# Kernel tuning notes

Hardware: AMD Instinct MI355X
Metric: run time of the kernel (lower is better)

Reference implementation:

```python
import jax, jax.numpy as jnp
import numpy as np

N = 100000
E = 1600000


def setup_inputs() -> dict:
    key = jax.random.key(0)
    ks = jax.random.split(key, 8)
    x = jax.random.normal(ks[0], (N, 4), dtype=jnp.float32)
    edge_index = jax.random.randint(ks[1], (2, E), 0, N)
    # Glorot-ish scaled weights
    W1 = jax.random.normal(ks[2], (4, 64), dtype=jnp.float32) / np.sqrt(4.0)
    b1 = jnp.zeros((64,), dtype=jnp.float32)
    W2 = jax.random.normal(ks[3], (64, 32), dtype=jnp.float32) / np.sqrt(64.0)
    b2 = jnp.zeros((32,), dtype=jnp.float32)
    Wf = jax.random.normal(ks[4], (32, 32), dtype=jnp.float32) / np.sqrt(32.0)
    bf = jnp.zeros((32,), dtype=jnp.float32)
    return {"x": x, "edge_index": edge_index, "W1": W1, "b1": b1,
            "W2": W2, "b2": b2, "Wf": Wf, "bf": bf}


def _gcn_conv(x, W, b, src, dst, n):
    """PyG GCNConv: out = D^{-1/2}(A+I)D^{-1/2} (x @ W) + b, sum-aggregated at dst."""
    h = x @ W  # [n, out] -- linear before propagate, like PyG
    # degree over dst (self-loops already appended in src/dst)
    deg = jax.ops.segment_sum(jnp.ones_like(dst, dtype=h.dtype), dst, num_segments=n)
    dinv = jnp.where(deg > 0, jax.lax.rsqrt(jnp.maximum(deg, 1.0)), 0.0)
    norm = dinv[src] * dinv[dst]  # [E+n]
    msg = h[src] * norm[:, None]  # gather + scale
    out = jax.ops.segment_sum(msg, dst, num_segments=n)  # scatter-add
    return out + b


def reference(x, edge_index, W1, b1, W2, b2, Wf, bf):
    n = x.shape[0]
    loops = jnp.arange(n, dtype=edge_index.dtype)
    src = jnp.concatenate([edge_index[0], loops])
    dst = jnp.concatenate([edge_index[1], loops])
    h = jax.nn.relu(_gcn_conv(x, W1, b1, src, dst, n))
    h = jax.nn.relu(_gcn_conv(h, W2, b2, src, dst, n))
    return jax.nn.relu(h @ Wf + bf)
```

## Files before the change

kernel.cpp:

```cpp
#include <hip/hip_runtime.h>
#include <hip/hip_fp16.h>


#define STRIDE 64
#define BSHIFT 7
#define CH 4096
#define PBS 1024
#define PT (CH / PBS)

__global__ __launch_bounds__(PBS) void k_place(const int* __restrict__ src,
                                               const int* __restrict__ dst,
                                               int* __restrict__ gcur,
                                               int* __restrict__ ebuf,
                                               int NB, int CAP, int E) {
    __shared__ int stage[CH];
    __shared__ unsigned short stageb[CH];
    __shared__ int histA[1024];
    __shared__ int gbaseL[1024];
    __shared__ int wtot[16];
    const int tid = threadIdx.x;
    const int base = blockIdx.x * CH;
    const int blkcnt = min(CH, E - base);

    histA[tid] = 0;
    __syncthreads();

    int posr[PT];
    unsigned short bkr[PT];
    unsigned char lnr[PT];
#pragma unroll
    for (int k = 0; k < PT; ++k) {
        int e = base + tid + k * PBS;
        if (e < E) {
            int d = dst[e];
            int b = d >> BSHIFT;
            bkr[k] = (unsigned short)b;
            lnr[k] = (unsigned char)(d & 127);
            posr[k] = atomicAdd(&histA[b], 1);
        }
    }
    __syncthreads();

    {
        int lane = tid & 63, wid = tid >> 6;
        int v = histA[tid];
#pragma unroll
        for (int o = 1; o < 64; o <<= 1) {
            int t2 = __shfl_up(v, o, 64);
            if (lane >= o) v += t2;
        }
        if (lane == 63) wtot[wid] = v;
        __syncthreads();
        int wpre = 0;
        for (int ww = 0; ww < wid; ++ww) wpre += wtot[ww];
        histA[tid] = v + wpre;
    }
    __syncthreads();

    int* A = histA;

    if (tid < NB) {
        int st = tid ? A[tid - 1] : 0;
        int cnt = A[tid] - st;
        gbaseL[tid] = cnt ? atomicAdd(&gcur[tid], cnt) : 0;
    }
    __syncthreads();

#pragma unroll
    for (int k = 0; k < PT; ++k) {
        int e = base + tid + k * PBS;
        if (e < E) {
            int b = bkr[k];
            int st = b ? A[b - 1] : 0;
            int idx = st + posr[k];
            stage[idx] = src[e] | ((int)lnr[k] << 17);
            stageb[idx] = (unsigned short)b;
        }
    }
    __syncthreads();

    for (int j = tid; j < blkcnt; j += PBS) {
        int b = stageb[j];
        int st = b ? A[b - 1] : 0;
        int o = gbaseL[b] + (j - st);
        if (o < CAP) ebuf[(size_t)b * CAP + o] = stage[j];
    }
}

__global__ __launch_bounds__(512) void k_fillsorted2(const int* __restrict__ ebuf,
                                                     const int* __restrict__ gcur,
                                                     int* __restrict__ adjF,
                                                     int* __restrict__ deg,
                                                     float* __restrict__ dinv,
                                                     const float4* __restrict__ x,
                                                     float4* __restrict__ xd,
                                                     int CAP, int N) {
    __shared__ int adjL[128 * STRIDE];
    __shared__ int cnt[128];
    const int b = blockIdx.x, tid = threadIdx.x;
    if (tid < 128) cnt[tid] = 0;
    __syncthreads();

    int count = min(gcur[b], CAP);
    const int* eb = ebuf + (size_t)b * CAP;
    for (int j = tid; j < count; j += 512) {
        int v = eb[j];
        int ln = (v >> 17) & 127;
        int s = v & 0x1FFFF;
        int slot = atomicAdd(&cnt[ln], 1);
        if (slot < STRIDE) adjL[(ln << 6) | slot] = s;
    }
    __syncthreads();

    const size_t gbase = (size_t)b << 13;
    for (int j = tid; j < 128 * STRIDE; j += 512) adjF[gbase + j] = adjL[j];

    if (tid < 128) {
        int node = (b << BSHIFT) + tid;
        if (node < N) {
            int k = cnt[tid];
            deg[node] = k;
            float di = rsqrtf((float)(k + 1));
            dinv[node] = di;
            float4 xv = x[node];
            xv.x *= di; xv.y *= di; xv.z *= di; xv.w *= di;
            xd[node] = xv;
        }
    }
}

__global__ void k_agg(const int* __restrict__ deg, const int* __restrict__ adjF,
                      const float4* __restrict__ xd, float4* __restrict__ aggx, int n) {
    int hw = blockIdx.x * (blockDim.x >> 5) + (threadIdx.x >> 5);
    int lane = threadIdx.x & 31;
    int sub = lane >> 3;
    int sl  = lane & 7;
    int node = hw * 4 + sub;
    bool valid = node < n;
    int nd = valid ? node : 0;
    int c = valid ? min(deg[nd], STRIDE) : 0;
    const int* row = adjF + ((size_t)nd << 6);

    float ax = 0.f, ay = 0.f, az = 0.f, aw = 0.f;
    int kk = sl;
    for (; kk + 8 < c; kk += 16) {
        int s0 = row[kk], s1 = row[kk + 8];
        float4 v0 = xd[s0];
        float4 v1 = xd[s1];
        ax += v0.x + v1.x; ay += v0.y + v1.y;
        az += v0.z + v1.z; aw += v0.w + v1.w;
    }
    if (kk < c) {
        float4 v = xd[row[kk]];
        ax += v.x; ay += v.y; az += v.z; aw += v.w;
    }
#pragma unroll
    for (int m = 4; m >= 1; m >>= 1) {
        ax += __shfl_xor(ax, m, 8);
        ay += __shfl_xor(ay, m, 8);
        az += __shfl_xor(az, m, 8);
        aw += __shfl_xor(aw, m, 8);
    }
    if (valid && sl == 0) aggx[nd] = make_float4(ax, ay, az, aw);
}

__global__ void k_mlp(const float4* __restrict__ aggx, const float4* __restrict__ xd,
                      const float* __restrict__ dinv,
                      const float* __restrict__ W1, const float* __restrict__ b1,
                      const float* __restrict__ W2, signed char* __restrict__ Qq,
                      float* __restrict__ Qs, int n) {
    int i = blockIdx.x * blockDim.x + threadIdx.x;
    if (i >= n) return;
    float4 s = aggx[i];
    float4 self = xd[i];
    float di = dinv[i];
    float ax = (s.x + self.x) * di, ay = (s.y + self.y) * di;
    float az = (s.z + self.z) * di, aw = (s.w + self.w) * di;

    float r[32];
#pragma unroll
    for (int c = 0; c < 32; ++c) r[c] = 0.0f;

#pragma unroll 8
    for (int j = 0; j < 64; ++j) {
        float h = fmaf(ax, W1[j], fmaf(ay, W1[64 + j],
                  fmaf(az, W1[128 + j], fmaf(aw, W1[192 + j], b1[j]))));
        h = fmaxf(h, 0.0f);
#pragma unroll
        for (int c = 0; c < 32; ++c) r[c] = fmaf(h, W2[j * 32 + c], r[c]);
    }

    float rm = 1e-12f;
#pragma unroll
    for (int c = 0; c < 32; ++c) {
        r[c] *= di;
        rm = fmaxf(rm, fabsf(r[c]));
    }
    float inv = 127.0f / rm;
    unsigned pk[8];
#pragma unroll
    for (int g = 0; g < 8; ++g) {
        unsigned q0 = (unsigned)(__float2int_rn(r[4 * g + 0] * inv)) & 0xFFu;
        unsigned q1 = (unsigned)(__float2int_rn(r[4 * g + 1] * inv)) & 0xFFu;
        unsigned q2 = (unsigned)(__float2int_rn(r[4 * g + 2] * inv)) & 0xFFu;
        unsigned q3 = (unsigned)(__float2int_rn(r[4 * g + 3] * inv)) & 0xFFu;
        pk[g] = q0 | (q1 << 8) | (q2 << 16) | (q3 << 24);
    }
    uint4* qq = (uint4*)(Qq + ((size_t)i << 5));
    qq[0] = make_uint4(pk[0], pk[1], pk[2], pk[3]);
    qq[1] = make_uint4(pk[4], pk[5], pk[6], pk[7]);
    Qs[i] = rm * (1.0f / 127.0f);
}

__global__ void k_final(const int* __restrict__ deg, const int* __restrict__ adjF,
                        const float* __restrict__ dinv,
                        const signed char* __restrict__ Qq,
                        const float* __restrict__ Qs, const float* __restrict__ b2,
                        const float* __restrict__ Wf, const float* __restrict__ bf,
                        float* __restrict__ out, int n) {
    int node = blockIdx.x * (blockDim.x >> 5) + (threadIdx.x >> 5);
    int lane = threadIdx.x & 31;
    bool valid = node < n;
    int nd = valid ? node : 0;
    int c = valid ? min(deg[nd], STRIDE) : 0;
    const int* row = adjF + ((size_t)nd << 6);
    const int nb = lane >> 3;
    const int cw = lane & 7;

    float a0 = 0.f, a1 = 0.f, a2 = 0.f, a3 = 0.f;
    for (int k = 0; k < c; k += 8) {
        int i0 = k + nb, i1 = k + 4 + nb;
        int s0 = row[min(i0, c - 1)];
        int s1 = row[min(i1, c - 1)];
        int w0 = ((const int*)(Qq + ((size_t)s0 << 5)))[cw];
        int w1 = ((const int*)(Qq + ((size_t)s1 << 5)))[cw];
        float sc0 = Qs[s0];
        float sc1 = Qs[s1];
        sc0 = (i0 < c) ? sc0 : 0.0f;
        sc1 = (i1 < c) ? sc1 : 0.0f;
        a0 = fmaf(sc0, (float)((signed char)(w0)), a0);
        a1 = fmaf(sc0, (float)((signed char)(w0 >> 8)), a1);
        a2 = fmaf(sc0, (float)((signed char)(w0 >> 16)), a2);
        a3 = fmaf(sc0, (float)(w0 >> 24), a3);
        a0 = fmaf(sc1, (float)((signed char)(w1)), a0);
        a1 = fmaf(sc1, (float)((signed char)(w1 >> 8)), a1);
        a2 = fmaf(sc1, (float)((signed char)(w1 >> 16)), a2);
        a3 = fmaf(sc1, (float)(w1 >> 24), a3);
    }

    a0 += __shfl_xor(a0, 8, 32);  a0 += __shfl_xor(a0, 16, 32);
    a1 += __shfl_xor(a1, 8, 32);  a1 += __shfl_xor(a1, 16, 32);
    a2 += __shfl_xor(a2, 8, 32);  a2 += __shfl_xor(a2, 16, 32);
    a3 += __shfl_xor(a3, 8, 32);  a3 += __shfl_xor(a3, 16, 32);

    int srcl = lane >> 2;
    float t0 = __shfl(a0, srcl, 32);
    float t1 = __shfl(a1, srcl, 32);
    float t2 = __shfl(a2, srcl, 32);
    float t3 = __shfl(a3, srcl, 32);
    int r2 = lane & 3;
    float accv = (r2 & 1) ? t1 : t0;
    float hi   = (r2 & 1) ? t3 : t2;
    accv = (r2 & 2) ? hi : accv;

    accv += Qs[nd] * (float)Qq[((size_t)nd << 5) | lane];

    float h = fmaxf(fmaf(accv, dinv[nd], b2[lane]), 0.0f);
    float o = bf[lane];
#pragma unroll
    for (int cc = 0; cc < 32; ++cc) {
        o = fmaf(__shfl(h, cc, 32), Wf[cc * 32 + lane], o);
    }
    if (valid) out[((size_t)node << 5) | lane] = fmaxf(o, 0.0f);
}

static inline size_t align_up(size_t x, size_t a) { return (x + a - 1) & ~(a - 1); }

extern "C" void kernel_launch(void* const* d_in, const int* in_sizes, int n_in,
                              void* d_out, int out_size, void* d_ws, size_t ws_size,
                              hipStream_t stream) {
    const int N = in_sizes[0] / 4;
    const int E = in_sizes[1] / 2;

    const float* x  = (const float*)d_in[0];
    const int*   ei = (const int*)d_in[1];
    const int*   src = ei;
    const int*   dst = ei + E;
    const float* W1 = (const float*)d_in[2];
    const float* b1 = (const float*)d_in[3];
    const float* W2 = (const float*)d_in[4];
    const float* b2 = (const float*)d_in[5];
    const float* Wf = (const float*)d_in[6];
    const float* bf = (const float*)d_in[7];
    float* out = (float*)d_out;

    const int NB  = (N + 127) >> BSHIFT;
    const int CAP = ((E + NB - 1) / NB) * 5 / 4 + 64;

    char* w = (char*)d_ws;
    size_t off = 0;
    int*    gcur = (int*)(w + off);         off += align_up((size_t)NB * 4, 256);
    int*    deg  = (int*)(w + off);         off += align_up((size_t)N * 4, 256);
    float*  dinv = (float*)(w + off);       off += align_up((size_t)N * 4, 256);
    float*  xd   = (float*)(w + off);       off += align_up((size_t)N * 16, 256);
    float*  aggx = (float*)(w + off);       off += align_up((size_t)N * 16, 256);
    int*    adjF = (int*)(w + off);         off += align_up((size_t)NB * 128 * STRIDE * 4, 256);
    signed char* Qq = (signed char*)(w + off); off += align_up((size_t)N * 32, 256);
    float*  Qs   = (float*)(w + off);       off += align_up((size_t)N * 4, 256);
    int*    ebuf = (int*)(w + off);         off += align_up((size_t)NB * CAP * 4, 256);

    const int B = 256;
    const int nplace = (E + CH - 1) / CH;

    hipMemsetAsync(gcur, 0, (size_t)NB * 4, stream);
    k_place<<<nplace, PBS, 0, stream>>>(src, dst, gcur, ebuf, NB, CAP, E);
    k_fillsorted2<<<NB, 512, 0, stream>>>(ebuf, gcur, adjF, deg, dinv,
                                          (const float4*)x, (float4*)xd, CAP, N);
    k_agg<<<(N + 31) / 32, B, 0, stream>>>(deg, adjF, (const float4*)xd,
                                           (float4*)aggx, N);
    k_mlp<<<(N + B - 1) / B, B, 0, stream>>>((const float4*)aggx, (const float4*)xd,
                                             dinv, W1, b1, W2, Qq, Qs, N);
    k_final<<<((size_t)N * 32 + B - 1) / B, B, 0, stream>>>(deg, adjF, dinv, Qq, Qs,
                                                            b2, Wf, bf, out, N);
}
```

Measured before the change: 170.6 us.

## Fuse aggregation and MLP kernels via shared memory; unroll final gather loop

Merges the first-layer neighbor aggregation and the per-node MLP/quantization into one kernel, passing aggregated features through shared memory instead of a global aggx buffer, which removes a launch and a global round-trip. Only 64 of 512 threads run the MLP phase, so that phase has low parallelism per block. The final gather kernel processes four neighbors per iteration and hoists per-node loads before the loop to raise memory-level parallelism.

```diff
diff --git a/kernel.cpp b/kernel.cpp
--- a/kernel.cpp
+++ b/kernel.cpp
@@ -129,13 +129,22 @@
     }
 }
 
-__global__ void k_agg(const int* __restrict__ deg, const int* __restrict__ adjF,
-                      const float4* __restrict__ xd, float4* __restrict__ aggx, int n) {
-    int hw = blockIdx.x * (blockDim.x >> 5) + (threadIdx.x >> 5);
-    int lane = threadIdx.x & 31;
-    int sub = lane >> 3;
-    int sl  = lane & 7;
-    int node = hw * 4 + sub;
+__global__ __launch_bounds__(512) void k_aggmlp(const int* __restrict__ deg,
+                                                const int* __restrict__ adjF,
+                                                const float4* __restrict__ xd,
+                                                const float* __restrict__ dinv,
+                                                const float* __restrict__ W1,
+                                                const float* __restrict__ b1,
+                                                const float* __restrict__ W2,
+                                                signed char* __restrict__ Qq,
+                                                float* __restrict__ Qs, int n) {
+    __shared__ float4 aggL[64];
+    const int tid = threadIdx.x;
+    const int lane = tid & 31;
+    const int sub = lane >> 3;
+    const int sl  = lane & 7;
+    const int nib = (tid >> 5) * 4 + sub;
+    const int node = blockIdx.x * 64 + nib;
     bool valid = node < n;
     int nd = valid ? node : 0;
     int c = valid ? min(deg[nd], STRIDE) : 0;
@@ -161,55 +170,53 @@
         az += __shfl_xor(az, m, 8);
         aw += __shfl_xor(aw, m, 8);
     }
-    if (valid && sl == 0) aggx[nd] = make_float4(ax, ay, az, aw);
-}
-
-__global__ void k_mlp(const float4* __restrict__ aggx, const float4* __restrict__ xd,
-                      const float* __restrict__ dinv,
-                      const float* __restrict__ W1, const float* __restrict__ b1,
-                      const float* __restrict__ W2, signed char* __restrict__ Qq,
-                      float* __restrict__ Qs, int n) {
-    int i = blockIdx.x * blockDim.x + threadIdx.x;
-    if (i >= n) return;
-    float4 s = aggx[i];
-    float4 self = xd[i];
-    float di = dinv[i];
-    float ax = (s.x + self.x) * di, ay = (s.y + self.y) * di;
-    float az = (s.z + self.z) * di, aw = (s.w + self.w) * di;
-
-    float r[32];
-#pragma unroll
-    for (int c = 0; c < 32; ++c) r[c] = 0.0f;
+    if (sl == 0) aggL[nib] = make_float4(ax, ay, az, aw);
+    __syncthreads();
+
+    if (tid < 64) {
+        int i = blockIdx.x * 64 + tid;
+        if (i < n) {
+            float4 s = aggL[tid];
+            float4 self = xd[i];
+            float di = dinv[i];
+            float bx = (s.x + self.x) * di, by = (s.y + self.y) * di;
+            float bz = (s.z + self.z) * di, bw = (s.w + self.w) * di;
+
+            float r[32];
+#pragma unroll
+            for (int cc = 0; cc < 32; ++cc) r[cc] = 0.0f;
 
 #pragma unroll 8
-    for (int j = 0; j < 64; ++j) {
-        float h = fmaf(ax, W1[j], fmaf(ay, W1[64 + j],
-                  fmaf(az, W1[128 + j], fmaf(aw, W1[192 + j], b1[j]))));
-        h = fmaxf(h, 0.0f);
-#pragma unroll
-        for (int c = 0; c < 32; ++c) r[c] = fmaf(h, W2[j * 32 + c], r[c]);
-    }
-
-    float rm = 1e-12f;
-#pragma unroll
-    for (int c = 0; c < 32; ++c) {
-        r[c] *= di;
-        rm = fmaxf(rm, fabsf(r[c]));
-    }
-    float inv = 127.0f / rm;
-    unsigned pk[8];
-#pragma unroll
-    for (int g = 0; g < 8; ++g) {
-        unsigned q0 = (unsigned)(__float2int_rn(r[4 * g + 0] * inv)) & 0xFFu;
-        unsigned q1 = (unsigned)(__float2int_rn(r[4 * g + 1] * inv)) & 0xFFu;
-        unsigned q2 = (unsigned)(__float2int_rn(r[4 * g + 2] * inv)) & 0xFFu;
-        unsigned q3 = (unsigned)(__float2int_rn(r[4 * g + 3] * inv)) & 0xFFu;
-        pk[g] = q0 | (q1 << 8) | (q2 << 16) | (q3 << 24);
-    }
-    uint4* qq = (uint4*)(Qq + ((size_t)i << 5));
-    qq[0] = make_uint4(pk[0], pk[1], pk[2], pk[3]);
-    qq[1] = make_uint4(pk[4], pk[5], pk[6], pk[7]);
-    Qs[i] = rm * (1.0f / 127.0f);
+            for (int j = 0; j < 64; ++j) {
+                float h = fmaf(bx, W1[j], fmaf(by, W1[64 + j],
+                          fmaf(bz, W1[128 + j], fmaf(bw, W1[192 + j], b1[j]))));
+                h = fmaxf(h, 0.0f);
+#pragma unroll
+                for (int cc = 0; cc < 32; ++cc) r[cc] = fmaf(h, W2[j * 32 + cc], r[cc]);
+            }
+
+            float rm = 1e-12f;
+#pragma unroll
+            for (int cc = 0; cc < 32; ++cc) {
+                r[cc] *= di;
+                rm = fmaxf(rm, fabsf(r[cc]));
+            }
+            float inv = 127.0f / rm;
+            unsigned pk[8];
+#pragma unroll
+            for (int g = 0; g < 8; ++g) {
+                unsigned q0 = (unsigned)(__float2int_rn(r[4 * g + 0] * inv)) & 0xFFu;
+                unsigned q1 = (unsigned)(__float2int_rn(r[4 * g + 1] * inv)) & 0xFFu;
+                unsigned q2 = (unsigned)(__float2int_rn(r[4 * g + 2] * inv)) & 0xFFu;
+                unsigned q3 = (unsigned)(__float2int_rn(r[4 * g + 3] * inv)) & 0xFFu;
+                pk[g] = q0 | (q1 << 8) | (q2 << 16) | (q3 << 24);
+            }
+            uint4* qq = (uint4*)(Qq + ((size_t)i << 5));
+            qq[0] = make_uint4(pk[0], pk[1], pk[2], pk[3]);
+            qq[1] = make_uint4(pk[4], pk[5], pk[6], pk[7]);
+            Qs[i] = rm * (1.0f / 127.0f);
+        }
+    }
 }
 
 __global__ void k_final(const int* __restrict__ deg, const int* __restrict__ adjF,
@@ -227,17 +234,30 @@
     const int nb = lane >> 3;
     const int cw = lane & 7;
 
+    float di   = dinv[nd];
+    float bb2  = b2[lane];
+    float bbf  = bf[lane];
+    float qself = Qs[nd] * (float)Qq[((size_t)nd << 5) | lane];
+
     float a0 = 0.f, a1 = 0.f, a2 = 0.f, a3 = 0.f;
-    for (int k = 0; k < c; k += 8) {
-        int i0 = k + nb, i1 = k + 4 + nb;
+    for (int k = 0; k < c; k += 16) {
+        int i0 = k + nb, i1 = k + 4 + nb, i2 = k + 8 + nb, i3 = k + 12 + nb;
         int s0 = row[min(i0, c - 1)];
         int s1 = row[min(i1, c - 1)];
+        int s2 = row[min(i2, c - 1)];
+        int s3 = row[min(i3, c - 1)];
         int w0 = ((const int*)(Qq + ((size_t)s0 << 5)))[cw];
         int w1 = ((const int*)(Qq + ((size_t)s1 << 5)))[cw];
+        int w2 = ((const int*)(Qq + ((size_t)s2 << 5)))[cw];
+        int w3 = ((const int*)(Qq + ((size_t)s3 << 5)))[cw];
         float sc0 = Qs[s0];
         float sc1 = Qs[s1];
+        float sc2 = Qs[s2];
+        float sc3 = Qs[s3];
         sc0 = (i0 < c) ? sc0 : 0.0f;
         sc1 = (i1 < c) ? sc1 : 0.0f;
+        sc2 = (i2 < c) ? sc2 : 0.0f;
+        sc3 = (i3 < c) ? sc3 : 0.0f;
         a0 = fmaf(sc0, (float)((signed char)(w0)), a0);
         a1 = fmaf(sc0, (float)((signed char)(w0 >> 8)), a1);
         a2 = fmaf(sc0, (float)((signed char)(w0 >> 16)), a2);
@@ -246,6 +266,14 @@
         a1 = fmaf(sc1, (float)((signed char)(w1 >> 8)), a1);
         a2 = fmaf(sc1, (float)((signed char)(w1 >> 16)), a2);
         a3 = fmaf(sc1, (float)(w1 >> 24), a3);
+        a0 = fmaf(sc2, (float)((signed char)(w2)), a0);
+        a1 = fmaf(sc2, (float)((signed char)(w2 >> 8)), a1);
+        a2 = fmaf(sc2, (float)((signed char)(w2 >> 16)), a2);
+        a3 = fmaf(sc2, (float)(w2 >> 24), a3);
+        a0 = fmaf(sc3, (float)((signed char)(w3)), a0);
+        a1 = fmaf(sc3, (float)((signed char)(w3 >> 8)), a1);
+        a2 = fmaf(sc3, (float)((signed char)(w3 >> 16)), a2);
+        a3 = fmaf(sc3, (float)(w3 >> 24), a3);
     }
 
     a0 += __shfl_xor(a0, 8, 32);  a0 += __shfl_xor(a0, 16, 32);
@@ -263,10 +291,10 @@
     float hi   = (r2 & 1) ? t3 : t2;
     accv = (r2 & 2) ? hi : accv;
 
-    accv += Qs[nd] * (float)Qq[((size_t)nd << 5) | lane];
-
-    float h = fmaxf(fmaf(accv, dinv[nd], b2[lane]), 0.0f);
-    float o = bf[lane];
+    accv += qself;
+
+    float h = fmaxf(fmaf(accv, di, bb2), 0.0f);
+    float o = bbf;
 #pragma unroll
     for (int cc = 0; cc < 32; ++cc) {
         o = fmaf(__shfl(h, cc, 32), Wf[cc * 32 + lane], o);
@@ -303,7 +331,6 @@
     int*    deg  = (int*)(w + off);         off += align_up((size_t)N * 4, 256);
     float*  dinv = (float*)(w + off);       off += align_up((size_t)N * 4, 256);
     float*  xd   = (float*)(w + off);       off += align_up((size_t)N * 16, 256);
-    float*  aggx = (float*)(w + off);       off += align_up((size_t)N * 16, 256);
     int*    adjF = (int*)(w + off);         off += align_up((size_t)NB * 128 * STRIDE * 4, 256);
     signed char* Qq = (signed char*)(w + off); off += align_up((size_t)N * 32, 256);
     float*  Qs   = (float*)(w + off);       off += align_up((size_t)N * 4, 256);
@@ -316,10 +343,8 @@
     k_place<<<nplace, PBS, 0, stream>>>(src, dst, gcur, ebuf, NB, CAP, E);
     k_fillsorted2<<<NB, 512, 0, stream>>>(ebuf, gcur, adjF, deg, dinv,
                                           (const float4*)x, (float4*)xd, CAP, N);
-    k_agg<<<(N + 31) / 32, B, 0, stream>>>(deg, adjF, (const float4*)xd,
-                                           (float4*)aggx, N);
-    k_mlp<<<(N + B - 1) / B, B, 0, stream>>>((const float4*)aggx, (const float4*)xd,
-                                             dinv, W1, b1, W2, Qq, Qs, N);
+    k_aggmlp<<<(N + 63) / 64, 512, 0, stream>>>(deg, adjF, (const float4*)xd,
+                                                dinv, W1, b1, W2, Qq, Qs, N);
     k_final<<<((size_t)N * 32 + B - 1) / B, B, 0, stream>>>(deg, adjF, dinv, Qq, Qs,
                                                             b2, Wf, bf, out, N);
 }
```

Result: faster. 158.9 us (-6.9%).
